# Performance work log

Hardware: AMD Instinct MI355X
Metric: run time of the kernel (lower is better)

Reference implementation:

```python
import jax, jax.numpy as jnp
import numpy as np

EMBED_DIM = 400
NUM_HEADS = 4
HEAD_SIZE = EMBED_DIM // NUM_HEADS  # 100


def setup_inputs() -> dict:
    key = jax.random.key(0)
    ks = jax.random.split(key, 6)
    B, T = 8, 2048
    x = jax.random.normal(ks[0], (B, T, EMBED_DIM), dtype=jnp.float32)
    # per-head projection weights, stacked over heads: [H, C, D]
    scale = 1.0 / np.sqrt(EMBED_DIM)
    Wq = jax.random.normal(ks[1], (NUM_HEADS, EMBED_DIM, HEAD_SIZE), dtype=jnp.float32) * scale
    Wk = jax.random.normal(ks[2], (NUM_HEADS, EMBED_DIM, HEAD_SIZE), dtype=jnp.float32) * scale
    Wv = jax.random.normal(ks[3], (NUM_HEADS, EMBED_DIM, HEAD_SIZE), dtype=jnp.float32) * scale
    Wo = jax.random.normal(ks[4], (EMBED_DIM, EMBED_DIM), dtype=jnp.float32) * scale
    bo = jax.random.normal(ks[5], (EMBED_DIM,), dtype=jnp.float32) * scale
    return {"x": x, "Wq": Wq, "Wk": Wk, "Wv": Wv, "Wo": Wo, "bo": bo}


def reference(x, Wq, Wk, Wv, Wo, bo):
    B, T, C = x.shape
    inv_sqrt_d = 1.0 / jnp.sqrt(jnp.asarray(HEAD_SIZE, x.dtype))
    # project: [B,T,C] x [H,C,D] -> [B,H,T,D]
    q = jnp.einsum('btc,hcd->bhtd', x, Wq)
    k = jnp.einsum('btc,hcd->bhtd', x, Wk)
    v = jnp.einsum('btc,hcd->bhtd', x, Wv)
    scores = jnp.einsum('bhtd,bhsd->bhts', q, k) * inv_sqrt_d  # [B,H,T,T]
    causal = jnp.tril(jnp.ones((T, T), dtype=bool))
    scores = jnp.where(causal, scores, -jnp.inf)
    attn = jax.nn.softmax(scores, axis=-1)
    out = jnp.einsum('bhts,bhsd->bhtd', attn, v)  # [B,H,T,D]
    # concat heads (head order matches torch concat on last dim)
    out = out.transpose(0, 2, 1, 3).reshape(B, T, C)
    # output projection; dropout is identity in eval mode
    return out @ Wo.T + bo
```

## Files before the change

### kernel.cpp

```cpp
#include <hip/hip_runtime.h>
#include <hip/hip_bf16.h>

#define B_ 8
#define T_ 2048
#define C_ 400
#define H_ 4
#define D_ 100
#define DP 128
#define KP 416
#define KPB 832
#define QSCALE 0.14426950408889634f
#define MSTATIC 16.0f

typedef __hip_bfloat16 bf16;
typedef unsigned int uint32;
typedef __attribute__((ext_vector_type(8))) short short8;
typedef __attribute__((ext_vector_type(4))) float f32x4;

__device__ __forceinline__ float bf2f(bf16 v){ return __bfloat162float(v); }
__device__ __forceinline__ bf16 f2bf(float f){ return __float2bfloat16(f); }
__device__ __forceinline__ unsigned short bfbits(float f){
  bf16 h = f2bf(f);
  return __builtin_bit_cast(unsigned short, h);
}
__device__ __forceinline__ uint32 pk2(float a, float b){
  return (uint32)bfbits(a) | ((uint32)bfbits(b) << 16);
}
__device__ __forceinline__ void gl_lds16(const char* gsrc, char* ldst){
  __builtin_amdgcn_global_load_lds(
      (const __attribute__((address_space(1))) unsigned int*)gsrc,
      (__attribute__((address_space(3))) unsigned int*)ldst, 16, 0, 0);
}

__global__ __launch_bounds__(256) void prep_all_kernel(const float* __restrict__ x,
    const float* __restrict__ Wq, const float* __restrict__ Wk,
    const float* __restrict__ Wv, const float* __restrict__ Wo,
    bf16* __restrict__ xb, bf16* __restrict__ WT, bf16* __restrict__ WoB){
  int i = blockIdx.x*256 + threadIdx.x;
  if (i < 16384*52){
    int c8 = i % 52, t = i / 52;
    uint32 u[4];
    if (c8 < 50){
      const float* src = x + (size_t)t*C_ + c8*8;
      #pragma unroll
      for (int k=0;k<4;++k) u[k] = pk2(src[2*k], src[2*k+1]);
    } else {
      u[0]=u[1]=u[2]=u[3]=0;
    }
    *reinterpret_cast<uint4*>((char*)xb + (size_t)t*KPB + c8*16) = make_uint4(u[0],u[1],u[2],u[3]);
    return;
  }
  i -= 16384*52;
  if (i < 12*128*KP){
    int c = i % KP, n = (i/KP) & 127, group = i/(KP*128);
    int p = group >> 2, h = group & 3;
    float v = 0.f;
    if (n < D_ && c < C_){
      const float* W = (p==0)?Wq:(p==1)?Wk:Wv;
      v = W[((size_t)h*C_ + c)*D_ + n];
    }
    WT[i] = f2bf(v);
    return;
  }
  i -= 12*128*KP;
  if (i < 512*KP){
    int c = i % KP, n = i / KP;
    float v = (n < C_ && c < C_) ? Wo[(size_t)n*C_ + c] : 0.f;
    WoB[i] = f2bf(v);
  }
}

__global__ __launch_bounds__(256) void qkv_gemm_kernel(const bf16* __restrict__ xb,
    const bf16* __restrict__ WT, bf16* __restrict__ Qp, bf16* __restrict__ Kp,
    bf16* __restrict__ VT){
  __shared__ __align__(16) char xs[2][8192];
  __shared__ __align__(16) char wsh[2][8192];
  int bid = blockIdx.x;
  int xcd = bid & 7, idx = bid >> 3;
  int mb = xcd*16 + idx/12;
  int group = idx % 12;
  int p = group >> 2, h = group & 3;
  int t0 = mb * 128;
  int tid = threadIdx.x;
  int w = tid >> 6, l = tid & 63, g = l >> 4, qi = l & 15;
  const char* xg = (const char*)xb + (size_t)t0*KPB;
  const char* wg = (const char*)WT + (size_t)group*128*KPB;
  int srow = tid >> 2, sseg = tid & 3;

  #define GSTAGE(J, BUF) {                                                     \
    int kc2 = (J)*64;                                                          \
    _Pragma("unroll")                                                          \
    for (int r2=0;r2<2;++r2)                                                   \
      gl_lds16(xg + (size_t)(srow + r2*64)*KPB + kc2 + sseg*16,                \
               &xs[BUF][tid*16 + r2*4096]);                                    \
    _Pragma("unroll")                                                          \
    for (int r2=0;r2<2;++r2)                                                   \
      gl_lds16(wg + (size_t)(srow + r2*64)*KPB + kc2 + sseg*16,                \
               &wsh[BUF][tid*16 + r2*4096]); }

  f32x4 acc[2][8];
  #pragma unroll
  for (int mt=0;mt<2;++mt)
    #pragma unroll
    for (int nt=0;nt<8;++nt) acc[mt][nt] = (f32x4){0.f,0.f,0.f,0.f};

  GSTAGE(0, 0)
  __syncthreads();
  for (int j = 0; j < 13; ++j){
    int cur = j & 1;
    if (j < 12) GSTAGE(j+1, cur^1)
    short8 af[2];
    #pragma unroll
    for (int mt=0;mt<2;++mt)
      af[mt] = *reinterpret_cast<const short8*>(&xs[cur][(w*32 + mt*16 + qi)*64 + g*16]);
    short8 bfr[8];
    #pragma unroll
    for (int nt=0;nt<8;++nt)
      bfr[nt] = *reinterpret_cast<const short8*>(&wsh[cur][(nt*16 + qi)*64 + g*16]);
    if (p < 2){
      #pragma unroll
      for (int mt=0;mt<2;++mt)
        #pragma unroll
        for (int nt=0;nt<8;++nt)
          acc[mt][nt] = __builtin_amdgcn_mfma_f32_16x16x32_bf16(af[mt], bfr[nt], acc[mt][nt], 0,0,0);
    } else {
      #pragma unroll
      for (int mt=0;mt<2;++mt)
        #pragma unroll
        for (int nt=0;nt<8;++nt)
          acc[mt][nt] = __builtin_amdgcn_mfma_f32_16x16x32_bf16(bfr[nt], af[mt], acc[mt][nt], 0,0,0);
    }
    __syncthreads();
  }

  int b = t0 >> 11, tloc0 = t0 & 2047;
  size_t bh = (size_t)b*H_ + h;
  if (p < 2){
    float qs = (p==0) ? QSCALE : 1.0f;
    bf16* dst = (p==0 ? Qp : Kp) + (bh*T_ + tloc0)*DP;
    #pragma unroll
    for (int mt=0;mt<2;++mt)
      #pragma unroll
      for (int r=0;r<4;++r){
        int tr = w*32 + mt*16 + 4*g + r;
        #pragma unroll
        for (int nt=0;nt<8;++nt)
          dst[(size_t)tr*DP + nt*16 + qi] = f2bf(qs * acc[mt][nt][r]);
      }
  } else {
    bf16* dstv = VT + bh*DP*T_ + tloc0;
    #pragma unroll
    for (int nt=0;nt<8;++nt)
      #pragma unroll
      for (int r=0;r<4;++r){
        int d = nt*16 + 4*g + r;
        #pragma unroll
        for (int mt=0;mt<2;++mt)
          dstv[(size_t)d*T_ + w*32 + mt*16 + qi] = f2bf(acc[mt][nt][r]);
      }
  }
  #undef GSTAGE
}

__global__ __launch_bounds__(256) void out_gemm_kernel(const bf16* __restrict__ AOb,
    const bf16* __restrict__ WoB, const float* __restrict__ bo, float* __restrict__ out){
  __shared__ __align__(16) char xs[2][8192];
  __shared__ __align__(16) char wsh[2][8192];
  int bid = blockIdx.x;
  int xcd = bid & 7, idx = bid >> 3;
  int mb = xcd*16 + idx/4;
  int nb = idx & 3;
  int t0 = mb * 128, n0 = nb * 128;
  int tid = threadIdx.x;
  int w = tid >> 6, l = tid & 63, g = l >> 4, qi = l & 15;
  const char* xg = (const char*)AOb + (size_t)t0*KPB;
  const char* wg = (const char*)WoB + (size_t)n0*KPB;
  int srow = tid >> 2, sseg = tid & 3;

  #define GSTAGE(J, BUF) {                                                     \
    int kc2 = (J)*64;                                                          \
    _Pragma("unroll")                                                          \
    for (int r2=0;r2<2;++r2)                                                   \
      gl_lds16(xg + (size_t)(srow + r2*64)*KPB + kc2 + sseg*16,                \
               &xs[BUF][tid*16 + r2*4096]);                                    \
    _Pragma("unroll")                                                          \
    for (int r2=0;r2<2;++r2)                                                   \
      gl_lds16(wg + (size_t)(srow + r2*64)*KPB + kc2 + sseg*16,                \
               &wsh[BUF][tid*16 + r2*4096]); }

  f32x4 acc[2][8];
  #pragma unroll
  for (int mt=0;mt<2;++mt)
    #pragma unroll
    for (int nt=0;nt<8;++nt) acc[mt][nt] = (f32x4){0.f,0.f,0.f,0.f};

  GSTAGE(0, 0)
  __syncthreads();
  for (int j = 0; j < 13; ++j){
    int cur = j & 1;
    if (j < 12) GSTAGE(j+1, cur^1)
    short8 af[2];
    #pragma unroll
    for (int mt=0;mt<2;++mt)
      af[mt] = *reinterpret_cast<const short8*>(&xs[cur][(w*32 + mt*16 + qi)*64 + g*16]);
    short8 bfr[8];
    #pragma unroll
    for (int nt=0;nt<8;++nt)
      bfr[nt] = *reinterpret_cast<const short8*>(&wsh[cur][(nt*16 + qi)*64 + g*16]);
    #pragma unroll
    for (int mt=0;mt<2;++mt)
      #pragma unroll
      for (int nt=0;nt<8;++nt)
        acc[mt][nt] = __builtin_amdgcn_mfma_f32_16x16x32_bf16(af[mt], bfr[nt], acc[mt][nt], 0,0,0);
    __syncthreads();
  }

  #pragma unroll
  for (int nt=0;nt<8;++nt){
    if (n0 + nt*16 >= C_) continue;
    int n = n0 + nt*16 + qi;
    float bv = bo[n];
    #pragma unroll
    for (int mt=0;mt<2;++mt)
      #pragma unroll
      for (int r=0;r<4;++r){
        int tr = w*32 + mt*16 + 4*g + r;
        out[(size_t)(t0 + tr)*C_ + n] = acc[mt][nt][r] + bv;
      }
  }
  #undef GSTAGE
}

__global__ __launch_bounds__(256, 2) void attn_kernel(const bf16* __restrict__ Qp,
    const bf16* __restrict__ Kp, const bf16* __restrict__ VT, bf16* __restrict__ AOb){
  __shared__ __align__(16) char ktile[2][16384];
  __shared__ __align__(16) char vtile[2][14336];
  __shared__ __align__(16) uint32 pshare[4*2*16*36];
  const float NEGINF = -__builtin_inff();
  int bid = blockIdx.x;
  int xcd = bid & 7, idx = bid >> 3;
  int bh  = xcd*4 + (idx & 3);
  int pr  = idx >> 2;
  int qbA = pr, qbB = 31 - pr;
  int tid = threadIdx.x;
  int w = tid >> 6, l = tid & 63;
  int g = l >> 4, qi = l & 15;
  int q0A = qbA*64 + w*16, q0B = qbB*64 + w*16;
  int nchA = qbA + 1, nchB = qbB + 1;

  const bf16* Qbase = Qp + (size_t)bh*T_*DP + g*8;
  const char* Kg    = (const char*)(Kp + (size_t)bh*T_*DP);
  const char* Vg    = (const char*)(VT + (size_t)bh*DP*T_);

  short8 qfA[4], qfB[4];
  #pragma unroll
  for (int ks=0; ks<4; ++ks){
    qfA[ks] = *reinterpret_cast<const short8*>(Qbase + (size_t)(q0A + qi)*DP + ks*32);
    qfB[ks] = *reinterpret_cast<const short8*>(Qbase + (size_t)(q0B + qi)*DP + ks*32);
  }

  f32x4 accA[7], accB[7];
  #pragma unroll
  for (int dt=0; dt<7; ++dt){
    accA[dt] = (f32x4){0.f,0.f,0.f,0.f};
    accB[dt] = (f32x4){0.f,0.f,0.f,0.f};
  }
  float lrA = 0.f, lrB = 0.f;

  uint32* pbB = &pshare[((w*2 + 0)*16 + qi)*36];
  uint32* pbA = &pshare[((w*2 + 1)*16 + qi)*36];

  int st_off0 = w*4096 + l*16;
  #define STAGE(J, BUF) { int k0s = (J) << 6;                                   \
    _Pragma("unroll")                                                           \
    for (int it=0; it<4; ++it){                                                 \
      int off = st_off0 + it*1024;                                              \
      int row = off >> 8;                                                       \
      int cb  = off & 255;                                                      \
      gl_lds16(Kg + (size_t)(k0s + row)*256 + (cb ^ ((row&15)<<4)),             \
               &ktile[BUF][w*4096 + it*1024]); } }

  #define VSTAGE(J, BUF) { int k0s2 = ((J) << 6)*2;                             \
    for (int it=w; it<14; it+=4){                                               \
      int off = it*1024 + l*16;                                                 \
      int row = off >> 7;                                                       \
      int cb  = off & 127;                                                      \
      gl_lds16(Vg + (size_t)row*(T_*2) + k0s2 + (cb ^ ((row&7)<<4)),            \
               &vtile[BUF][it*1024 + l*16]); } }

  auto softpack = [&](const f32x4 st[4], float& lr, int qglob, int k0,
                      bool maskch, uint32* pb){
    float p[4][4];
    if (maskch){
      #pragma unroll
      for (int kt=0; kt<4; ++kt)
        #pragma unroll
        for (int r=0; r<4; ++r){
          int key = k0 + kt*16 + 4*g + r;
          float v = st[kt][r]; if (key > qglob) v = NEGINF;
          p[kt][r] = exp2f(v - MSTATIC);
        }
    } else {
      #pragma unroll
      for (int kt=0; kt<4; ++kt)
        #pragma unroll
        for (int r=0; r<4; ++r)
          p[kt][r] = exp2f(st[kt][r] - MSTATIC);
    }
    float rs = 0.f;
    #pragma unroll
    for (int kt=0; kt<4; ++kt)
      #pragma unroll
      for (int r=0; r<4; ++r) rs += p[kt][r];
    lr += rs;
    #pragma unroll
    for (int kt=0; kt<4; ++kt){
      pb[kt*8 + 2*g    ] = pk2(p[kt][0], p[kt][1]);
      pb[kt*8 + 2*g + 1] = pk2(p[kt][2], p[kt][3]);
    }
  };

  STAGE(0, 0)
  VSTAGE(0, 0)
  __syncthreads();

  for (int j = 0; j < nchB; ++j){
    int k0 = j << 6;
    int cur = j & 1;
    if (j + 1 < nchB){ STAGE(j+1, cur^1) VSTAGE(j+1, cur^1) }
    const char* kb = ktile[cur];
    const char* vb = vtile[cur];
    bool dual = (j < nchA);
    f32x4 stA[4], stB[4];
    __builtin_amdgcn_s_setprio(1);
    #pragma unroll
    for (int kt=0; kt<4; ++kt){
      f32x4 sB = (f32x4){0.f,0.f,0.f,0.f};
      f32x4 sA = (f32x4){0.f,0.f,0.f,0.f};
      #pragma unroll
      for (int ks=0; ks<4; ++ks){
        short8 kf = *reinterpret_cast<const short8*>(
            kb + (kt*16 + qi)*256 + ((ks*64 + g*16) ^ (qi<<4)));
        sB = __builtin_amdgcn_mfma_f32_16x16x32_bf16(kf, qfB[ks], sB, 0, 0, 0);
        if (dual)
          sA = __builtin_amdgcn_mfma_f32_16x16x32_bf16(kf, qfA[ks], sA, 0, 0, 0);
      }
      stB[kt] = sB; stA[kt] = sA;
    }
    __builtin_amdgcn_s_setprio(0);
    softpack(stB, lrB, q0B + qi, k0, j == nchB - 1, pbB);
    if (dual)
      softpack(stA, lrA, q0A + qi, k0, j == nchA - 1, pbA);
    __builtin_amdgcn_s_setprio(1);
    #pragma unroll
    for (int ks=0; ks<2; ++ks){
      short8 paB = *reinterpret_cast<const short8*>(pbB + 16*ks + 4*g);
      short8 paA = *reinterpret_cast<const short8*>(pbA + 16*ks + 4*g);
      #pragma unroll
      for (int dt=0; dt<7; ++dt){
        int row = dt*16 + qi;
        short8 vf = *reinterpret_cast<const short8*>(
            vb + row*128 + ((ks*64 + g*16) ^ ((qi&7)<<4)));
        accB[dt] = __builtin_amdgcn_mfma_f32_16x16x32_bf16(paB, vf, accB[dt], 0, 0, 0);
        if (dual)
          accA[dt] = __builtin_amdgcn_mfma_f32_16x16x32_bf16(paA, vf, accA[dt], 0, 0, 0);
      }
    }
    __builtin_amdgcn_s_setprio(0);
    __syncthreads();
  }

  lrA += __shfl_xor(lrA, 16); lrA += __shfl_xor(lrA, 32);
  lrB += __shfl_xor(lrB, 16); lrB += __shfl_xor(lrB, 32);

  int b = bh >> 2, h = bh & 3;
  #pragma unroll
  for (int tix=0; tix<2; ++tix){
    f32x4* acc = tix ? accA : accB;
    float lr = tix ? lrA : lrB;
    int q0 = tix ? q0A : q0B;
    float inv = 1.f / lr;
    float invr[4];
    #pragma unroll
    for (int r=0; r<4; ++r) invr[r] = __shfl(inv, 20*g + r);
    #pragma unroll
    for (int dt=0; dt<7; ++dt){
      int d = dt*16 + qi;
      if (d < D_){
        #pragma unroll
        for (int r=0; r<4; ++r){
          size_t row = (size_t)(b*T_) + q0 + 4*g + r;
          AOb[row*KP + h*D_ + d] = f2bf(acc[dt][r] * invr[r]);
        }
      }
    }
  }
  #undef STAGE
  #undef VSTAGE
}

extern "C" void kernel_launch(void* const* d_in, const int* in_sizes, int n_in,
                              void* d_out, int out_size, void* d_ws, size_t ws_size,
                              hipStream_t stream){
  const float* x  = (const float*)d_in[0];
  const float* Wq = (const float*)d_in[1];
  const float* Wk = (const float*)d_in[2];
  const float* Wv = (const float*)d_in[3];
  const float* Wo = (const float*)d_in[4];
  const float* bo = (const float*)d_in[5];

  constexpr size_t NBH  = (size_t)B_*H_;
  constexpr size_t NPAD = NBH*T_*DP;
  constexpr size_t NROW = (size_t)B_*T_;
  constexpr size_t OFF_QP  = 0;
  constexpr size_t OFF_KP  = OFF_QP + NPAD*2;
  constexpr size_t OFF_VT  = OFF_KP + NPAD*2;
  constexpr size_t OFF_XB  = OFF_VT + NPAD*2;
  constexpr size_t OFF_AOB = OFF_XB + NROW*KP*2;
  constexpr size_t OFF_WT  = OFF_AOB + NROW*KP*2;
  constexpr size_t OFF_WOB = OFF_WT + (size_t)12*128*KP*2;
  constexpr size_t TOTAL   = OFF_WOB + (size_t)512*KP*2;
  if (ws_size < TOTAL) return;

  char* ws = (char*)d_ws;
  bf16*  Qp   = (bf16*)(ws + OFF_QP);
  bf16*  Kp   = (bf16*)(ws + OFF_KP);
  bf16*  VTp  = (bf16*)(ws + OFF_VT);
  bf16*  xb   = (bf16*)(ws + OFF_XB);
  bf16*  AOb  = (bf16*)(ws + OFF_AOB);
  bf16*  WT   = (bf16*)(ws + OFF_WT);
  bf16*  WoB  = (bf16*)(ws + OFF_WOB);
  float* out  = (float*)d_out;

  constexpr int PREP_N = 16384*52 + 12*128*KP + 512*KP;
  prep_all_kernel<<<(PREP_N + 255)/256, 256, 0, stream>>>(x, Wq, Wk, Wv, Wo, xb, WT, WoB);
  qkv_gemm_kernel<<<1536, 256, 0, stream>>>(xb, WT, Qp, Kp, VTp);
  attn_kernel<<<512, 256, 0, stream>>>(Qp, Kp, VTp, AOb);
  out_gemm_kernel<<<512, 256, 0, stream>>>(AOb, WoB, bo, out);
}
```

Measured before the change: 141.7 us.

## Double QKV GEMM N-tile per block and read V directly from global in attention

The QKV projection now computes two weight groups (heads) per block, reusing each staged x tile for twice as many MFMAs and halving the grid. The attention kernel drops the LDS staging of V tiles and loads V fragments straight from global memory, freeing shared memory so launch bounds can request three blocks per CU. The risk is uncoalesced, unpipelined global V loads stalling the PV MFMAs, plus higher register pressure in the QKV kernel from doubled accumulators.

```diff
diff --git a/kernel.cpp b/kernel.cpp
--- a/kernel.cpp
+++ b/kernel.cpp
@@ -74,17 +74,19 @@
     const bf16* __restrict__ WT, bf16* __restrict__ Qp, bf16* __restrict__ Kp,
     bf16* __restrict__ VT){
   __shared__ __align__(16) char xs[2][8192];
-  __shared__ __align__(16) char wsh[2][8192];
+  __shared__ __align__(16) char wsh[2][2][8192];
   int bid = blockIdx.x;
   int xcd = bid & 7, idx = bid >> 3;
-  int mb = xcd*16 + idx/12;
-  int group = idx % 12;
-  int p = group >> 2, h = group & 3;
+  int mb = xcd*16 + idx/6;
+  int gpair = idx % 6;
+  int group0 = gpair*2;
+  int p = group0 >> 2;
   int t0 = mb * 128;
   int tid = threadIdx.x;
   int w = tid >> 6, l = tid & 63, g = l >> 4, qi = l & 15;
   const char* xg = (const char*)xb + (size_t)t0*KPB;
-  const char* wg = (const char*)WT + (size_t)group*128*KPB;
+  const char* wg0 = (const char*)WT + (size_t)group0*128*KPB;
+  const char* wg1 = wg0 + (size_t)128*KPB;
   int srow = tid >> 2, sseg = tid & 3;
 
   #define GSTAGE(J, BUF) {                                                     \
@@ -95,14 +97,20 @@
                &xs[BUF][tid*16 + r2*4096]);                                    \
     _Pragma("unroll")                                                          \
     for (int r2=0;r2<2;++r2)                                                   \
-      gl_lds16(wg + (size_t)(srow + r2*64)*KPB + kc2 + sseg*16,                \
-               &wsh[BUF][tid*16 + r2*4096]); }
-
-  f32x4 acc[2][8];
-  #pragma unroll
-  for (int mt=0;mt<2;++mt)
-    #pragma unroll
-    for (int nt=0;nt<8;++nt) acc[mt][nt] = (f32x4){0.f,0.f,0.f,0.f};
+      gl_lds16(wg0 + (size_t)(srow + r2*64)*KPB + kc2 + sseg*16,               \
+               &wsh[BUF][0][tid*16 + r2*4096]);                                \
+    _Pragma("unroll")                                                          \
+    for (int r2=0;r2<2;++r2)                                                   \
+      gl_lds16(wg1 + (size_t)(srow + r2*64)*KPB + kc2 + sseg*16,               \
+               &wsh[BUF][1][tid*16 + r2*4096]); }
+
+  f32x4 acc[2][2][8];
+  #pragma unroll
+  for (int gr=0;gr<2;++gr)
+    #pragma unroll
+    for (int mt=0;mt<2;++mt)
+      #pragma unroll
+      for (int nt=0;nt<8;++nt) acc[gr][mt][nt] = (f32x4){0.f,0.f,0.f,0.f};
 
   GSTAGE(0, 0)
   __syncthreads();
@@ -113,51 +121,58 @@
     #pragma unroll
     for (int mt=0;mt<2;++mt)
       af[mt] = *reinterpret_cast<const short8*>(&xs[cur][(w*32 + mt*16 + qi)*64 + g*16]);
-    short8 bfr[8];
-    #pragma unroll
-    for (int nt=0;nt<8;++nt)
-      bfr[nt] = *reinterpret_cast<const short8*>(&wsh[cur][(nt*16 + qi)*64 + g*16]);
+    #pragma unroll
+    for (int gr=0;gr<2;++gr){
+      short8 bfr[8];
+      #pragma unroll
+      for (int nt=0;nt<8;++nt)
+        bfr[nt] = *reinterpret_cast<const short8*>(&wsh[cur][gr][(nt*16 + qi)*64 + g*16]);
+      if (p < 2){
+        #pragma unroll
+        for (int mt=0;mt<2;++mt)
+          #pragma unroll
+          for (int nt=0;nt<8;++nt)
+            acc[gr][mt][nt] = __builtin_amdgcn_mfma_f32_16x16x32_bf16(af[mt], bfr[nt], acc[gr][mt][nt], 0,0,0);
+      } else {
+        #pragma unroll
+        for (int mt=0;mt<2;++mt)
+          #pragma unroll
+          for (int nt=0;nt<8;++nt)
+            acc[gr][mt][nt] = __builtin_amdgcn_mfma_f32_16x16x32_bf16(bfr[nt], af[mt], acc[gr][mt][nt], 0,0,0);
+      }
+    }
+    __syncthreads();
+  }
+
+  int b = t0 >> 11, tloc0 = t0 & 2047;
+  #pragma unroll
+  for (int gr=0;gr<2;++gr){
+    int h = (group0 + gr) & 3;
+    size_t bh = (size_t)b*H_ + h;
     if (p < 2){
+      float qs = (p==0) ? QSCALE : 1.0f;
+      bf16* dst = (p==0 ? Qp : Kp) + (bh*T_ + tloc0)*DP;
       #pragma unroll
       for (int mt=0;mt<2;++mt)
         #pragma unroll
-        for (int nt=0;nt<8;++nt)
-          acc[mt][nt] = __builtin_amdgcn_mfma_f32_16x16x32_bf16(af[mt], bfr[nt], acc[mt][nt], 0,0,0);
+        for (int r=0;r<4;++r){
+          int tr = w*32 + mt*16 + 4*g + r;
+          #pragma unroll
+          for (int nt=0;nt<8;++nt)
+            dst[(size_t)tr*DP + nt*16 + qi] = f2bf(qs * acc[gr][mt][nt][r]);
+        }
     } else {
-      #pragma unroll
-      for (int mt=0;mt<2;++mt)
-        #pragma unroll
-        for (int nt=0;nt<8;++nt)
-          acc[mt][nt] = __builtin_amdgcn_mfma_f32_16x16x32_bf16(bfr[nt], af[mt], acc[mt][nt], 0,0,0);
-    }
-    __syncthreads();
-  }
-
-  int b = t0 >> 11, tloc0 = t0 & 2047;
-  size_t bh = (size_t)b*H_ + h;
-  if (p < 2){
-    float qs = (p==0) ? QSCALE : 1.0f;
-    bf16* dst = (p==0 ? Qp : Kp) + (bh*T_ + tloc0)*DP;
-    #pragma unroll
-    for (int mt=0;mt<2;++mt)
-      #pragma unroll
-      for (int r=0;r<4;++r){
-        int tr = w*32 + mt*16 + 4*g + r;
-        #pragma unroll
-        for (int nt=0;nt<8;++nt)
-          dst[(size_t)tr*DP + nt*16 + qi] = f2bf(qs * acc[mt][nt][r]);
-      }
-  } else {
-    bf16* dstv = VT + bh*DP*T_ + tloc0;
-    #pragma unroll
-    for (int nt=0;nt<8;++nt)
-      #pragma unroll
-      for (int r=0;r<4;++r){
-        int d = nt*16 + 4*g + r;
-        #pragma unroll
-        for (int mt=0;mt<2;++mt)
-          dstv[(size_t)d*T_ + w*32 + mt*16 + qi] = f2bf(acc[mt][nt][r]);
-      }
+      bf16* dstv = VT + bh*DP*T_ + tloc0;
+      #pragma unroll
+      for (int nt=0;nt<8;++nt)
+        #pragma unroll
+        for (int r=0;r<4;++r){
+          int d = nt*16 + 4*g + r;
+          #pragma unroll
+          for (int mt=0;mt<2;++mt)
+            dstv[(size_t)d*T_ + w*32 + mt*16 + qi] = f2bf(acc[gr][mt][nt][r]);
+        }
+    }
   }
   #undef GSTAGE
 }
@@ -231,10 +246,9 @@
   #undef GSTAGE
 }
 
-__global__ __launch_bounds__(256, 2) void attn_kernel(const bf16* __restrict__ Qp,
+__global__ __launch_bounds__(256, 3) void attn_kernel(const bf16* __restrict__ Qp,
     const bf16* __restrict__ Kp, const bf16* __restrict__ VT, bf16* __restrict__ AOb){
   __shared__ __align__(16) char ktile[2][16384];
-  __shared__ __align__(16) char vtile[2][14336];
   __shared__ __align__(16) uint32 pshare[4*2*16*36];
   const float NEGINF = -__builtin_inff();
   int bid = blockIdx.x;
@@ -280,14 +294,6 @@
       gl_lds16(Kg + (size_t)(k0s + row)*256 + (cb ^ ((row&15)<<4)),             \
                &ktile[BUF][w*4096 + it*1024]); } }
 
-  #define VSTAGE(J, BUF) { int k0s2 = ((J) << 6)*2;                             \
-    for (int it=w; it<14; it+=4){                                               \
-      int off = it*1024 + l*16;                                                 \
-      int row = off >> 7;                                                       \
-      int cb  = off & 127;                                                      \
-      gl_lds16(Vg + (size_t)row*(T_*2) + k0s2 + (cb ^ ((row&7)<<4)),            \
-               &vtile[BUF][it*1024 + l*16]); } }
-
   auto softpack = [&](const f32x4 st[4], float& lr, int qglob, int k0,
                       bool maskch, uint32* pb){
     float p[4][4];
@@ -321,15 +327,13 @@
   };
 
   STAGE(0, 0)
-  VSTAGE(0, 0)
   __syncthreads();
 
   for (int j = 0; j < nchB; ++j){
     int k0 = j << 6;
     int cur = j & 1;
-    if (j + 1 < nchB){ STAGE(j+1, cur^1) VSTAGE(j+1, cur^1) }
+    if (j + 1 < nchB) STAGE(j+1, cur^1)
     const char* kb = ktile[cur];
-    const char* vb = vtile[cur];
     bool dual = (j < nchA);
     f32x4 stA[4], stB[4];
     __builtin_amdgcn_s_setprio(1);
@@ -358,9 +362,8 @@
       short8 paA = *reinterpret_cast<const short8*>(pbA + 16*ks + 4*g);
       #pragma unroll
       for (int dt=0; dt<7; ++dt){
-        int row = dt*16 + qi;
         short8 vf = *reinterpret_cast<const short8*>(
-            vb + row*128 + ((ks*64 + g*16) ^ ((qi&7)<<4)));
+            Vg + (size_t)(dt*16 + qi)*(T_*2) + (size_t)(k0 + ks*32 + g*8)*2);
         accB[dt] = __builtin_amdgcn_mfma_f32_16x16x32_bf16(paB, vf, accB[dt], 0, 0, 0);
         if (dual)
           accA[dt] = __builtin_amdgcn_mfma_f32_16x16x32_bf16(paA, vf, accA[dt], 0, 0, 0);
@@ -396,7 +399,6 @@
     }
   }
   #undef STAGE
-  #undef VSTAGE
 }
 
 extern "C" void kernel_launch(void* const* d_in, const int* in_sizes, int n_in,
@@ -434,7 +436,7 @@
 
   constexpr int PREP_N = 16384*52 + 12*128*KP + 512*KP;
   prep_all_kernel<<<(PREP_N + 255)/256, 256, 0, stream>>>(x, Wq, Wk, Wv, Wo, xb, WT, WoB);
-  qkv_gemm_kernel<<<1536, 256, 0, stream>>>(xb, WT, Qp, Kp, VTp);
+  qkv_gemm_kernel<<<768, 256, 0, stream>>>(xb, WT, Qp, Kp, VTp);
   attn_kernel<<<512, 256, 0, stream>>>(Qp, Kp, VTp, AOb);
   out_gemm_kernel<<<512, 256, 0, stream>>>(AOb, WoB, bo, out);
 }
```

After: 262.9 us. +85.5%, slower.
